# Kernel tuning notes

Measured on AMD Instinct MI355X. Metric: run time of the kernel, lower is better.

The kernel has to match this reference:

```python
import jax, jax.numpy as jnp
import numpy as np

L0, L1, L2 = 32, 16, 8
NS, NB = 512, 256
CUT = 7.0
N, E, G = 16384, 131072, 16
FEAT = L0 + 3 * L1 + 5 * L2  # 120


def setup_inputs() -> dict:
    key = jax.random.key(0)
    ks = jax.random.split(key, 16)
    rn = lambda k, s, sc=1.0: jax.random.normal(k, s, jnp.float32) * sc
    inp = {}
    inp['nodes'] = rn(ks[0], (N, FEAT))
    inp['pos'] = rn(ks[1], (N, 3)) * 5.0
    inp['cell'] = rn(ks[2], (G, 3, 3))
    inp['edge_shift'] = rn(ks[3], (E, 3))
    # tensor-product path weights (e3nn FullyConnectedTensorProduct, uvw mode)
    inp['W0'] = rn(ks[4], (L0, L0, NS))
    inp['W1'] = rn(ks[5], (L1, L1, NS))
    inp['W2'] = rn(ks[6], (L2, L2, NS))
    inp['ln_g'] = jnp.ones((NS,), jnp.float32)
    inp['ln_b'] = jnp.zeros((NS,), jnp.float32)
    inp['df_w1'] = rn(ks[7], (NB, 1024), NB ** -0.5)
    inp['df_b1'] = jnp.zeros((1024,), jnp.float32)
    inp['df_w2'] = rn(ks[8], (1024, NS), 1024 ** -0.5)
    inp['df_b2'] = jnp.zeros((NS,), jnp.float32)
    inp['mi_w1'] = rn(ks[9], (NS, 1024), NS ** -0.5)
    inp['mi_b1'] = jnp.zeros((1024,), jnp.float32)
    inp['mi_w2'] = rn(ks[10], (1024, 1024), 1024 ** -0.5)
    inp['mi_b2'] = jnp.zeros((1024,), jnp.float32)
    inp['mo_w'] = rn(ks[11], (1024, 1), 1024 ** -0.5)
    inp['mo_b'] = jnp.zeros((1,), jnp.float32)
    inp['edge_index'] = jax.random.randint(ks[12], (2, E), 0, N)
    inp['batch_vec'] = jnp.sort(jax.random.randint(ks[13], (N,), 0, G))
    return inp


def _split_irreps(x):
    x0 = x[:, :L0]                                   # (E, L0) scalars 0e
    x1 = x[:, L0:L0 + 3 * L1].reshape(-1, L1, 3)      # (E, L1, 3) vectors 1o
    x2 = x[:, L0 + 3 * L1:].reshape(-1, L2, 5)        # (E, L2, 5) 2e
    return x0, x1, x2


def reference(nodes, pos, cell, edge_shift, W0, W1, W2, ln_g, ln_b,
              df_w1, df_b1, df_w2, df_b2, mi_w1, mi_b1, mi_w2, mi_b2,
              mo_w, mo_b, edge_index, batch_vec):
    src, dst = edge_index[0], edge_index[1]
    # periodic-image translation vector per edge
    bcell = cell[batch_vec[src]]                      # (E,3,3)
    tvec = jnp.einsum('ei,eij->ej', edge_shift, bcell)
    radvec = pos[dst] - pos[src] + tvec               # (E,3)
    dist = jnp.linalg.norm(radvec, axis=1, keepdims=True)  # (E,1)
    r = 1.0 / (dist + 1e-6)
    # Bessel radial embedding with cutoff CUT, NB basis functions
    n = jnp.arange(1, NB + 1, dtype=jnp.float32)
    emb = jnp.sqrt(2.0 / CUT) * jnp.sin(n * jnp.pi * r / CUT) / r  # (E,NB)
    distfilter = jax.nn.silu(emb @ df_w1 + df_b1) @ df_w2 + df_b2  # (E,NS)

    # symmetrized fully-connected tensor product -> 0e scalars
    # 0.5*(tp(xs,xd)+tp(xd,xs)) == contraction of euv with symmetrized W
    xs0, xs1, xs2 = _split_irreps(nodes[src])
    xd0, xd1, xd2 = _split_irreps(nodes[dst])
    fan = jnp.sqrt(jnp.float32(L0 * L0 + L1 * L1 + L2 * L2))  # element path norm
    sym = lambda W: 0.5 * (W + W.transpose(1, 0, 2))
    e0 = jnp.einsum('eu,ev->euv', xs0, xd0)
    mixed = jnp.einsum('euv,uvw->ew', e0, sym(W0)) / fan
    e1 = jnp.einsum('eui,evi->euv', xs1, xd1)
    mixed = mixed + jnp.einsum('euv,uvw->ew', e1, sym(W1)) / (fan * jnp.sqrt(3.0))
    e2 = jnp.einsum('eui,evi->euv', xs2, xd2)
    mixed = mixed + jnp.einsum('euv,uvw->ew', e2, sym(W2)) / (fan * jnp.sqrt(5.0))

    # LayerNorm over numscalars
    mu = jnp.mean(mixed, axis=-1, keepdims=True)
    var = jnp.mean((mixed - mu) ** 2, axis=-1, keepdims=True)
    mixednorm = (mixed - mu) * jax.lax.rsqrt(var + 1e-5) * ln_g + ln_b

    reg = mixednorm * distfilter
    h = jax.nn.silu(reg @ mi_w1 + mi_b1)
    h = jax.nn.silu(h @ mi_w2 + mi_b2)
    return h @ mo_w + mo_b  # (E,1)
```

## Files before the change

kernel.cpp:

```cpp
#include <hip/hip_runtime.h>

#define EE 131072
#define NNODE 16384
#define FEAT 120
#define NS 512
#define NB 256
#define KCAT 1344

typedef unsigned short u16;
typedef __bf16 bf16x8 __attribute__((ext_vector_type(8)));
typedef float f32x4 __attribute__((ext_vector_type(4)));
typedef float f32x16 __attribute__((ext_vector_type(16)));
typedef unsigned short ushort8 __attribute__((ext_vector_type(8)));

__device__ __forceinline__ float b2f(u16 u) {
  union { unsigned int i; float f; } x; x.i = ((unsigned int)u) << 16; return x.f;
}
__device__ __forceinline__ u16 f2b(float f) {
  union { float f; unsigned int i; } x; x.f = f;
  unsigned int lsb = (x.i >> 16) & 1u;
  x.i += 0x7fffu + lsb;
  return (u16)(x.i >> 16);
}
__device__ __forceinline__ u16 f2b_fast(float f) {
  __bf16 h = (__bf16)f;
  union { __bf16 h; u16 u; } x; x.h = h; return x.u;
}
__device__ __forceinline__ float rdany(const void* p, long i, int f32) {
  return f32 ? ((const float*)p)[i] : b2f(((const u16*)p)[i]);
}

__device__ __forceinline__ void gload16(const u16* g, u16* l) {
  __builtin_amdgcn_global_load_lds(
      (__attribute__((address_space(1))) void*)(u16*)g,
      (__attribute__((address_space(3))) void*)l, 16, 0, 0);
}

__global__ void detect_k(const u16* __restrict__ nodes, int* __restrict__ flag) {
  __shared__ int cnt;
  if (threadIdx.x == 0) cnt = 0;
  __syncthreads();
  u16 v = nodes[threadIdx.x];
  int e = (v >> 7) & 0xFF;
  if (e >= 0x48) atomicAdd(&cnt, 1);
  __syncthreads();
  if (threadIdx.x == 0) *flag = (cnt >= 16) ? 1 : 0;
}

__global__ __launch_bounds__(256) void convert_k(const void* __restrict__ src,
                                                 u16* __restrict__ dst, long n,
                                                 const int* __restrict__ flag) {
  long i = (long)blockIdx.x * 256 + threadIdx.x;
  if (i >= n) return;
  if (*flag)
    dst[i] = f2b(((const float*)src)[i]);
  else
    dst[i] = ((const u16*)src)[i];
}

__global__ __launch_bounds__(256) void transpose_k(const u16* __restrict__ in,
                                                   u16* __restrict__ out, int R, int C) {
  __shared__ u16 tile[32][33];
  int c0 = blockIdx.x * 32, r0 = blockIdx.y * 32;
  int tx = threadIdx.x & 31, ty = threadIdx.x >> 5;
  for (int i = 0; i < 32; i += 8) {
    int r = r0 + ty + i, c = c0 + tx;
    if (r < R && c < C) tile[ty + i][tx] = in[(long)r * C + c];
  }
  __syncthreads();
  for (int i = 0; i < 32; i += 8) {
    int r = r0 + tx, c = c0 + ty + i;
    if (r < R && c < C) out[(long)c * R + r] = tile[tx][ty + i];
  }
}

__global__ __launch_bounds__(256) void build_wcat(const u16* __restrict__ W0,
                                                  const u16* __restrict__ W1,
                                                  const u16* __restrict__ W2,
                                                  u16* __restrict__ wcT) {
  int idx = blockIdx.x * 256 + threadIdx.x;
  if (idx >= NS * KCAT) return;
  int w = idx / KCAT, k = idx - w * KCAT;
  const float fan = 36.66060556f;
  float val;
  if (k < 1024) {
    int u = k >> 5, v = k & 31;
    val = 0.5f * (b2f(W0[(u * 32 + v) * NS + w]) + b2f(W0[(v * 32 + u) * NS + w])) / fan;
  } else if (k < 1280) {
    int j = k - 1024;
    int u = j >> 4, v = j & 15;
    val = 0.5f * (b2f(W1[(u * 16 + v) * NS + w]) + b2f(W1[(v * 16 + u) * NS + w])) /
          (fan * 1.7320508076f);
  } else {
    int j = k - 1280;
    int u = j >> 3, v = j & 7;
    val = 0.5f * (b2f(W2[(u * 8 + v) * NS + w]) + b2f(W2[(v * 8 + u) * NS + w])) /
          (fan * 2.2360679775f);
  }
  wcT[idx] = f2b(val);
}

__global__ __launch_bounds__(256) void edge_prep(
    const u16* __restrict__ nodes, const void* __restrict__ pos, const void* __restrict__ cell,
    const void* __restrict__ shift, const int* __restrict__ eidx, const int* __restrict__ batch,
    u16* __restrict__ emb, u16* __restrict__ ocat, int e0, const int* __restrict__ flag) {
  const int wave = threadIdx.x >> 6, lane = threadIdx.x & 63;
  const int el = blockIdx.x * 4 + wave;
  const int e = e0 + el;
  const int f32 = *flag;
  __shared__ u16 sxs[4][FEAT], sxd[4][FEAT];
  const int src = eidx[e], dst = eidx[EE + e];
  for (int i = lane; i < FEAT; i += 64) {
    sxs[wave][i] = nodes[(long)src * FEAT + i];
    sxd[wave][i] = nodes[(long)dst * FEAT + i];
  }
  __syncthreads();
  const int b = batch[src];
  float s0 = rdany(shift, (long)e * 3, f32), s1 = rdany(shift, (long)e * 3 + 1, f32),
        s2 = rdany(shift, (long)e * 3 + 2, f32);
  float d2 = 0.f;
#pragma unroll
  for (int j = 0; j < 3; j++) {
    float tv = s0 * rdany(cell, b * 9 + j, f32) + s1 * rdany(cell, b * 9 + 3 + j, f32) +
               s2 * rdany(cell, b * 9 + 6 + j, f32);
    float rv = rdany(pos, dst * 3 + j, f32) - rdany(pos, src * 3 + j, f32) + tv;
    d2 += rv * rv;
  }
  float dist = sqrtf(d2);
  float r = 1.0f / (dist + 1e-6f);
  const float c0 = 0.5345224838f;
  const float pi7 = 0.44879895051f;
#pragma unroll
  for (int j = 0; j < 4; j++) {
    int n = lane + 64 * j;
    float val = c0 * sinf((float)(n + 1) * pi7 * r) / r;
    emb[(long)el * NB + n] = f2b(val);
  }
  const u16* xs = sxs[wave];
  const u16* xd = sxd[wave];
  u16* orow = ocat + (long)el * KCAT;
#pragma unroll
  for (int j = 0; j < 16; j++) {
    int k = lane + 64 * j;
    int u = k >> 5, v = k & 31;
    orow[k] = f2b(b2f(xs[u]) * b2f(xd[v]));
  }
#pragma unroll
  for (int j = 0; j < 4; j++) {
    int k = lane + 64 * j;
    int u = k >> 4, v = k & 15;
    float s = 0.f;
#pragma unroll
    for (int i = 0; i < 3; i++) s += b2f(xs[32 + u * 3 + i]) * b2f(xd[32 + v * 3 + i]);
    orow[1024 + k] = f2b(s);
  }
  {
    int u = lane >> 3, v = lane & 7;
    float s = 0.f;
#pragma unroll
    for (int i = 0; i < 5; i++) s += b2f(xs[80 + u * 5 + i]) * b2f(xd[80 + v * 5 + i]);
    orow[1280 + lane] = f2b(s);
  }
}

template <int ACT, int OF32, int HEAD>
__global__ __launch_bounds__(256) void gemm_bt(const u16* __restrict__ A,
                                               const u16* __restrict__ BT,
                                               const u16* __restrict__ bias,
                                               void* __restrict__ Cv,
                                               const u16* __restrict__ hw,
                                               float* __restrict__ outf, int N, int K) {
  __shared__ __align__(16) u16 lA[128 * 64];
  __shared__ __align__(16) u16 lB[128 * 64];
  const int tid = threadIdx.x;
  const int wave = tid >> 6, lane = tid & 63;
  const int half = lane >> 5, l32 = lane & 31, r7 = lane & 7;

  const int nb_n = N >> 7;
  const int nb_m = gridDim.x / nb_n;
  int mi, ni;
  if ((nb_m & 7) == 0) {
    int f = blockIdx.x;
    int xcd = f & 7, s = f >> 3;
    int per = nb_m >> 3;
    mi = xcd * per + s / nb_n;
    ni = s - (s / nb_n) * nb_n;
  } else {
    mi = blockIdx.x / nb_n;
    ni = blockIdx.x - mi * nb_n;
  }
  const long m0 = (long)mi * 128;
  const int n0 = ni * 128;
  const int wm = (wave >> 1) * 64, wn = (wave & 1) * 64;

  f32x16 acc[2][2];
#pragma unroll
  for (int i = 0; i < 2; i++)
#pragma unroll
    for (int j = 0; j < 2; j++)
#pragma unroll
      for (int q = 0; q < 16; q++) acc[i][j][q] = 0.f;

  const int srow = tid >> 3;
  const int gseg = (tid & 7) ^ (srow & 7);
  const u16* Ag = A + (m0 + srow) * K + gseg * 8;
  const u16* Bg = BT + (long)(n0 + srow) * K + gseg * 8;
  u16* la = &lA[tid * 8];
  u16* lb = &lB[tid * 8];

  for (int k0 = 0; k0 < K; k0 += 64) {
#pragma unroll
    for (int ro = 0; ro < 4; ro++) gload16(Ag + (long)(ro * 32) * K + k0, la + ro * 2048);
#pragma unroll
    for (int ro = 0; ro < 4; ro++) gload16(Bg + (long)(ro * 32) * K + k0, lb + ro * 2048);
    __syncthreads();
#pragma unroll
    for (int s = 0; s < 4; s++) {
      const int sl = ((((s << 1) + half) ^ r7) << 3);
      bf16x8 a0 = *(const bf16x8*)&lA[(wm + l32) * 64 + sl];
      bf16x8 a1 = *(const bf16x8*)&lA[(wm + 32 + l32) * 64 + sl];
      bf16x8 b0 = *(const bf16x8*)&lB[(wn + l32) * 64 + sl];
      bf16x8 b1 = *(const bf16x8*)&lB[(wn + 32 + l32) * 64 + sl];
      acc[0][0] = __builtin_amdgcn_mfma_f32_32x32x16_bf16(a0, b0, acc[0][0], 0, 0, 0);
      acc[0][1] = __builtin_amdgcn_mfma_f32_32x32x16_bf16(a0, b1, acc[0][1], 0, 0, 0);
      acc[1][0] = __builtin_amdgcn_mfma_f32_32x32x16_bf16(a1, b0, acc[1][0], 0, 0, 0);
      acc[1][1] = __builtin_amdgcn_mfma_f32_32x32x16_bf16(a1, b1, acc[1][1], 0, 0, 0);
    }
    __syncthreads();
  }

  float* Cf = (float*)Cv;
  u16* Cb = (u16*)Cv;
  float rsum[2][16];
  if (HEAD) {
#pragma unroll
    for (int mt = 0; mt < 2; mt++)
#pragma unroll
      for (int rg = 0; rg < 16; rg++) rsum[mt][rg] = 0.f;
  }
#pragma unroll
  for (int mt = 0; mt < 2; mt++) {
#pragma unroll
    for (int nt = 0; nt < 2; nt++) {
      const int col = n0 + wn + nt * 32 + l32;
      float bv = bias ? b2f(bias[col]) : 0.0f;
      float hwv = HEAD ? b2f(hw[col]) : 0.f;
#pragma unroll
      for (int rg = 0; rg < 16; rg++) {
        long row = m0 + wm + mt * 32 + (rg & 3) + ((rg >> 2) << 3) + (half << 2);
        float v = acc[mt][nt][rg] + bv;
        if (ACT) v = __fdividef(v, 1.0f + __expf(-v));
        if (HEAD) {
          rsum[mt][rg] += v * hwv;
        } else if (OF32) {
          Cf[row * N + col] = v;
        } else {
          Cb[row * N + col] = f2b_fast(v);
        }
      }
    }
  }
  if (HEAD) {
#pragma unroll
    for (int mt = 0; mt < 2; mt++)
#pragma unroll
      for (int rg = 0; rg < 16; rg++) {
        float s = rsum[mt][rg];
        s += __shfl_xor(s, 1);
        s += __shfl_xor(s, 2);
        s += __shfl_xor(s, 4);
        s += __shfl_xor(s, 8);
        s += __shfl_xor(s, 16);
        if (l32 == 0) {
          long row = m0 + wm + mt * 32 + (rg & 3) + ((rg >> 2) << 3) + (half << 2);
          atomicAdd(&outf[row], s);
        }
      }
  }
}

__global__ __launch_bounds__(256) void ln_mul_k(const float* __restrict__ mixed,
                                                const u16* __restrict__ g,
                                                const u16* __restrict__ bvec,
                                                u16* __restrict__ dfreg) {
  const int wave = threadIdx.x >> 6, lane = threadIdx.x & 63;
  const long e = (long)blockIdx.x * 4 + wave;
  const float* row = mixed + e * NS;
  float x[8];
  f32x4 v0 = *(const f32x4*)&row[lane * 8];
  f32x4 v1 = *(const f32x4*)&row[lane * 8 + 4];
#pragma unroll
  for (int j = 0; j < 4; j++) { x[j] = v0[j]; x[4 + j] = v1[j]; }
  float s = 0.f, sq = 0.f;
#pragma unroll
  for (int j = 0; j < 8; j++) { s += x[j]; sq += x[j] * x[j]; }
  for (int o = 32; o; o >>= 1) { s += __shfl_xor(s, o); sq += __shfl_xor(sq, o); }
  float mu = s * (1.0f / 512.0f);
  float var = sq * (1.0f / 512.0f) - mu * mu;
  float rstd = rsqrtf(var + 1e-5f);
  u16* drow = dfreg + e * NS;
  ushort8 dv = *(const ushort8*)&drow[lane * 8];
  ushort8 ov;
#pragma unroll
  for (int j = 0; j < 8; j++) {
    int c = lane * 8 + j;
    float val = (x[j] - mu) * rstd * b2f(g[c]) + b2f(bvec[c]);
    ov[j] = f2b(val * b2f(dv[j]));
  }
  *(ushort8*)&drow[lane * 8] = ov;
}

__global__ __launch_bounds__(256) void head_finish(const float* __restrict__ outf,
                                                   const u16* __restrict__ b,
                                                   void* __restrict__ out,
                                                   const int* __restrict__ flag) {
  int e = blockIdx.x * 256 + threadIdx.x;
  float v = outf[e] + b2f(b[0]);
  if (*flag)
    ((float*)out)[e] = v;
  else
    ((u16*)out)[e] = f2b(v);
}

extern "C" void kernel_launch(void* const* d_in, const int* in_sizes, int n_in, void* d_out,
                              int out_size, void* d_ws, size_t ws_size, hipStream_t stream) {
  const int* eidx = (const int*)d_in[19];
  const int* batch = (const int*)d_in[20];

  char* ws = (char*)d_ws;
  size_t off = 0;
  auto alloc = [&](size_t bytes) {
    char* p = ws + off;
    off += (bytes + 255) & ~(size_t)255;
    return p;
  };

  int* flag = (int*)alloc(256);
  float* outf = (float*)alloc((size_t)EE * 4);

  detect_k<<<1, 256, 0, stream>>>((const u16*)d_in[0], flag);

  u16* cv[19];
  for (int i = 0; i < 19; i++) {
    long n = in_sizes[i];
    cv[i] = (u16*)alloc((size_t)n * 2);
    convert_k<<<(int)((n + 255) / 256), 256, 0, stream>>>(d_in[i], cv[i], n, flag);
  }
  const u16* nodes = cv[0];
  const u16* W0 = cv[4];
  const u16* W1 = cv[5];
  const u16* W2 = cv[6];
  const u16* ln_g = cv[7];
  const u16* ln_b = cv[8];
  const u16* df_w1 = cv[9];
  const u16* df_b1 = cv[10];
  const u16* df_w2 = cv[11];
  const u16* df_b2 = cv[12];
  const u16* mi_w1 = cv[13];
  const u16* mi_b1 = cv[14];
  const u16* mi_w2 = cv[15];
  const u16* mi_b2 = cv[16];
  const u16* mo_w = cv[17];
  const u16* mo_b = cv[18];

  u16* w1T = (u16*)alloc(1024 * 256 * 2);
  u16* w2T = (u16*)alloc(512 * 1024 * 2);
  u16* m1T = (u16*)alloc(1024 * 512 * 2);
  u16* m2T = (u16*)alloc((size_t)1024 * 1024 * 2);
  u16* wcT = (u16*)alloc((size_t)NS * KCAT * 2);

  int nchunk = 1;
  while (nchunk < 64) {
    size_t CHs = (size_t)(EE / nchunk);
    size_t need = off + CHs * 6272 + 8192;
    if (need <= ws_size) break;
    nchunk <<= 1;
  }
  const int CH = EE / nchunk;

  u16* ocat = (u16*)alloc((size_t)CH * KCAT * 2);
  u16* emb = (u16*)alloc((size_t)CH * NB * 2);
  u16* h1 = (u16*)alloc((size_t)CH * 1024 * 2);
  u16* dfb = (u16*)alloc((size_t)CH * NS * 2);
  u16* h2 = ocat;
  float* mixed = (float*)h1;

  transpose_k<<<dim3(1024 / 32, 256 / 32), 256, 0, stream>>>(df_w1, w1T, 256, 1024);
  transpose_k<<<dim3(512 / 32, 1024 / 32), 256, 0, stream>>>(df_w2, w2T, 1024, 512);
  transpose_k<<<dim3(1024 / 32, 512 / 32), 256, 0, stream>>>(mi_w1, m1T, 512, 1024);
  transpose_k<<<dim3(1024 / 32, 1024 / 32), 256, 0, stream>>>(mi_w2, m2T, 1024, 1024);
  build_wcat<<<(NS * KCAT + 255) / 256, 256, 0, stream>>>(W0, W1, W2, wcT);

  hipMemsetAsync(outf, 0, (size_t)EE * 4, stream);

  const int RB = CH / 128;
  for (int c = 0; c < nchunk; c++) {
    const int eb = c * CH;
    edge_prep<<<CH / 4, 256, 0, stream>>>(nodes, d_in[1], d_in[2], d_in[3], eidx, batch, emb,
                                          ocat, eb, flag);

    gemm_bt<1, 0, 0><<<RB * 8, 256, 0, stream>>>(emb, w1T, df_b1, h1, nullptr, nullptr, 1024, 256);
    gemm_bt<0, 0, 0><<<RB * 4, 256, 0, stream>>>(h1, w2T, df_b2, dfb, nullptr, nullptr, 512, 1024);

    gemm_bt<0, 1, 0><<<RB * 4, 256, 0, stream>>>(ocat, wcT, nullptr, mixed, nullptr, nullptr, 512,
                                                 1344);

    ln_mul_k<<<CH / 4, 256, 0, stream>>>(mixed, ln_g, ln_b, dfb);

    gemm_bt<1, 0, 0><<<RB * 8, 256, 0, stream>>>(dfb, m1T, mi_b1, h2, nullptr, nullptr, 1024, 512);
    gemm_bt<1, 0, 1><<<RB * 8, 256, 0, stream>>>(h2, m2T, mi_b2, nullptr, mo_w, outf + eb, 1024,
                                                 1024);
  }
  head_finish<<<EE / 256, 256, 0, stream>>>(outf, mo_b, d_out, flag);
}
```

Baseline: 1.651 ms.

## Rewrite GEMM as 256x256 tile, 8-wave, double-buffered pipelined MFMA kernel

Replaces the 128x128, 4-wave GEMM with a 256x256 tile computed by 8 waves. Each wave now holds a 128x64 accumulator. LDS is double-buffered and the A/B loads for the next K step are interleaved with MFMA phases, with s_setprio and explicit waitcnt and barriers. The XCD-aware block remap is simplified and the epilogue is adapted to the larger per-wave tile. This aims to raise data reuse per load and hide global latency behind compute. In exchange it uses much more LDS and registers per block, launches fewer blocks, and has intricate barrier ordering that could be fragile.

```diff
diff --git a/kernel.cpp b/kernel.cpp
--- a/kernel.cpp
+++ b/kernel.cpp
@@ -163,119 +163,205 @@
   }
 }
 
+#define STG_A(buf, h, kk)                                                        \
+  do {                                                                           \
+    gload16(Ag + ((h) * 128) * (long)K + (kk), &lA[buf][(h) * 8192 + tid * 8]);  \
+    gload16(Ag + ((h) * 128 + 64) * (long)K + (kk),                              \
+            &lA[buf][(h) * 8192 + 4096 + tid * 8]);                              \
+  } while (0)
+#define STG_B(buf, h, kk)                                                        \
+  do {                                                                           \
+    gload16(Bg + ((h) * 128) * (long)K + (kk), &lB[buf][(h) * 8192 + tid * 8]);  \
+    gload16(Bg + ((h) * 128 + 64) * (long)K + (kk),                              \
+            &lB[buf][(h) * 8192 + 4096 + tid * 8]);                              \
+  } while (0)
+#define RD_A(buf, fm, s)                                                         \
+  (*(const bf16x8*)&lA[buf][((wm * 128 + (fm)*32 + l32) << 6) +                  \
+                            ((((s)*2 + half) ^ r7) << 3)])
+#define RD_B(buf, fn, s)                                                         \
+  (*(const bf16x8*)&lB[buf][((wn * 64 + (fn)*32 + l32) << 6) +                   \
+                            ((((s)*2 + half) ^ r7) << 3)])
+#define MF(a, b, c) __builtin_amdgcn_mfma_f32_32x32x16_bf16(a, b, c, 0, 0, 0)
+
 template <int ACT, int OF32, int HEAD>
-__global__ __launch_bounds__(256) void gemm_bt(const u16* __restrict__ A,
-                                               const u16* __restrict__ BT,
-                                               const u16* __restrict__ bias,
-                                               void* __restrict__ Cv,
-                                               const u16* __restrict__ hw,
-                                               float* __restrict__ outf, int N, int K) {
-  __shared__ __align__(16) u16 lA[128 * 64];
-  __shared__ __align__(16) u16 lB[128 * 64];
+__global__ __launch_bounds__(512, 2) void gemm_bt(const u16* __restrict__ A,
+                                                  const u16* __restrict__ BT,
+                                                  const u16* __restrict__ bias,
+                                                  void* __restrict__ Cv,
+                                                  const u16* __restrict__ hw,
+                                                  float* __restrict__ outf, int N, int K) {
+  __shared__ __align__(16) u16 lA[2][256 * 64];
+  __shared__ __align__(16) u16 lB[2][256 * 64];
   const int tid = threadIdx.x;
-  const int wave = tid >> 6, lane = tid & 63;
+  const int lane = tid & 63;
+  const int wave = tid >> 6;
   const int half = lane >> 5, l32 = lane & 31, r7 = lane & 7;
-
-  const int nb_n = N >> 7;
-  const int nb_m = gridDim.x / nb_n;
-  int mi, ni;
-  if ((nb_m & 7) == 0) {
-    int f = blockIdx.x;
-    int xcd = f & 7, s = f >> 3;
-    int per = nb_m >> 3;
-    mi = xcd * per + s / nb_n;
-    ni = s - (s / nb_n) * nb_n;
-  } else {
-    mi = blockIdx.x / nb_n;
-    ni = blockIdx.x - mi * nb_n;
-  }
-  const long m0 = (long)mi * 128;
-  const int n0 = ni * 128;
-  const int wm = (wave >> 1) * 64, wn = (wave & 1) * 64;
-
-  f32x16 acc[2][2];
-#pragma unroll
-  for (int i = 0; i < 2; i++)
-#pragma unroll
-    for (int j = 0; j < 2; j++)
-#pragma unroll
-      for (int q = 0; q < 16; q++) acc[i][j][q] = 0.f;
+  const int wm = wave >> 2, wn = wave & 3;
+
+  const int nbn = N >> 8;
+  int idx = blockIdx.x;
+  if ((gridDim.x & 7) == 0) {
+    int per = gridDim.x >> 3;
+    idx = (blockIdx.x & 7) * per + (blockIdx.x >> 3);
+  }
+  const int mi = idx / nbn;
+  const int ni = idx - mi * nbn;
+  const long m0 = (long)mi * 256;
+  const int n0 = ni << 8;
+  const int nk = K >> 6;
 
   const int srow = tid >> 3;
   const int gseg = (tid & 7) ^ (srow & 7);
-  const u16* Ag = A + (m0 + srow) * K + gseg * 8;
+  const u16* Ag = A + (m0 + srow) * (long)K + gseg * 8;
   const u16* Bg = BT + (long)(n0 + srow) * K + gseg * 8;
-  u16* la = &lA[tid * 8];
-  u16* lb = &lB[tid * 8];
-
-  for (int k0 = 0; k0 < K; k0 += 64) {
-#pragma unroll
-    for (int ro = 0; ro < 4; ro++) gload16(Ag + (long)(ro * 32) * K + k0, la + ro * 2048);
-#pragma unroll
-    for (int ro = 0; ro < 4; ro++) gload16(Bg + (long)(ro * 32) * K + k0, lb + ro * 2048);
-    __syncthreads();
+
+  f32x16 acc[4][2];
+#pragma unroll
+  for (int i = 0; i < 4; i++)
+#pragma unroll
+    for (int j = 0; j < 2; j++)
+#pragma unroll
+      for (int q = 0; q < 16; q++) acc[i][j][q] = 0.f;
+
+  STG_A(0, 0, 0);
+  STG_A(0, 1, 0);
+  STG_B(0, 0, 0);
+  STG_B(0, 1, 0);
+  if (nk > 1) {
+    STG_B(1, 0, 64);
+    STG_B(1, 1, 64);
+    asm volatile("s_waitcnt vmcnt(4)" ::: "memory");
+  } else {
+    asm volatile("s_waitcnt vmcnt(0)" ::: "memory");
+  }
+  __builtin_amdgcn_s_barrier();
+
+  bf16x8 av[2][4], b0[4], b1[4];
+
+  for (int t = 0; t < nk; ++t) {
+    const int cur = t & 1, nxt = cur ^ 1;
+    const int kA = (t + 1) << 6;
+    const int kB = (t + 2) << 6;
+    const bool pA = (t + 1) < nk;
+    const bool pB = (t + 2) < nk;
+
 #pragma unroll
     for (int s = 0; s < 4; s++) {
-      const int sl = ((((s << 1) + half) ^ r7) << 3);
-      bf16x8 a0 = *(const bf16x8*)&lA[(wm + l32) * 64 + sl];
-      bf16x8 a1 = *(const bf16x8*)&lA[(wm + 32 + l32) * 64 + sl];
-      bf16x8 b0 = *(const bf16x8*)&lB[(wn + l32) * 64 + sl];
-      bf16x8 b1 = *(const bf16x8*)&lB[(wn + 32 + l32) * 64 + sl];
-      acc[0][0] = __builtin_amdgcn_mfma_f32_32x32x16_bf16(a0, b0, acc[0][0], 0, 0, 0);
-      acc[0][1] = __builtin_amdgcn_mfma_f32_32x32x16_bf16(a0, b1, acc[0][1], 0, 0, 0);
-      acc[1][0] = __builtin_amdgcn_mfma_f32_32x32x16_bf16(a1, b0, acc[1][0], 0, 0, 0);
-      acc[1][1] = __builtin_amdgcn_mfma_f32_32x32x16_bf16(a1, b1, acc[1][1], 0, 0, 0);
-    }
-    __syncthreads();
-  }
-
+      av[0][s] = RD_A(cur, 0, s);
+      av[1][s] = RD_A(cur, 1, s);
+      b0[s] = RD_B(cur, 0, s);
+    }
+    if (pA) STG_A(nxt, 0, kA);
+    __builtin_amdgcn_s_barrier();
+    asm volatile("s_waitcnt lgkmcnt(0)" ::: "memory");
+    __builtin_amdgcn_s_setprio(1);
+#pragma unroll
+    for (int s = 0; s < 4; s++) {
+      acc[0][0] = MF(av[0][s], b0[s], acc[0][0]);
+      acc[1][0] = MF(av[1][s], b0[s], acc[1][0]);
+    }
+    __builtin_amdgcn_s_setprio(0);
+    __builtin_amdgcn_s_barrier();
+
+#pragma unroll
+    for (int s = 0; s < 4; s++) b1[s] = RD_B(cur, 1, s);
+    if (pA) STG_A(nxt, 1, kA);
+    __builtin_amdgcn_s_barrier();
+    asm volatile("s_waitcnt lgkmcnt(0)" ::: "memory");
+    __builtin_amdgcn_s_setprio(1);
+#pragma unroll
+    for (int s = 0; s < 4; s++) {
+      acc[0][1] = MF(av[0][s], b1[s], acc[0][1]);
+      acc[1][1] = MF(av[1][s], b1[s], acc[1][1]);
+    }
+    __builtin_amdgcn_s_setprio(0);
+    __builtin_amdgcn_s_barrier();
+
+#pragma unroll
+    for (int s = 0; s < 4; s++) {
+      av[0][s] = RD_A(cur, 2, s);
+      av[1][s] = RD_A(cur, 3, s);
+    }
+    if (pB) STG_B(cur, 0, kB);
+    __builtin_amdgcn_s_barrier();
+    asm volatile("s_waitcnt lgkmcnt(0)" ::: "memory");
+    __builtin_amdgcn_s_setprio(1);
+#pragma unroll
+    for (int s = 0; s < 4; s++) {
+      acc[2][0] = MF(av[0][s], b0[s], acc[2][0]);
+      acc[3][0] = MF(av[1][s], b0[s], acc[3][0]);
+    }
+    __builtin_amdgcn_s_setprio(0);
+    __builtin_amdgcn_s_barrier();
+
+    if (pB) {
+      STG_B(cur, 1, kB);
+      asm volatile("s_waitcnt vmcnt(4)" ::: "memory");
+    } else {
+      asm volatile("s_waitcnt vmcnt(0)" ::: "memory");
+    }
+    __builtin_amdgcn_s_barrier();
+    __builtin_amdgcn_s_setprio(1);
+#pragma unroll
+    for (int s = 0; s < 4; s++) {
+      acc[2][1] = MF(av[0][s], b1[s], acc[2][1]);
+      acc[3][1] = MF(av[1][s], b1[s], acc[3][1]);
+    }
+    __builtin_amdgcn_s_setprio(0);
+    __builtin_amdgcn_s_barrier();
+  }
+
+  const int colb = n0 + wn * 64 + l32;
   float* Cf = (float*)Cv;
   u16* Cb = (u16*)Cv;
-  float rsum[2][16];
   if (HEAD) {
-#pragma unroll
-    for (int mt = 0; mt < 2; mt++)
-#pragma unroll
-      for (int rg = 0; rg < 16; rg++) rsum[mt][rg] = 0.f;
-  }
-#pragma unroll
-  for (int mt = 0; mt < 2; mt++) {
-#pragma unroll
-    for (int nt = 0; nt < 2; nt++) {
-      const int col = n0 + wn + nt * 32 + l32;
-      float bv = bias ? b2f(bias[col]) : 0.0f;
-      float hwv = HEAD ? b2f(hw[col]) : 0.f;
+    const float bv0 = b2f(bias[colb]), bv1 = b2f(bias[colb + 32]);
+    const float hw0 = b2f(hw[colb]), hw1 = b2f(hw[colb + 32]);
+#pragma unroll
+    for (int fm = 0; fm < 4; fm++) {
 #pragma unroll
       for (int rg = 0; rg < 16; rg++) {
-        long row = m0 + wm + mt * 32 + (rg & 3) + ((rg >> 2) << 3) + (half << 2);
-        float v = acc[mt][nt][rg] + bv;
-        if (ACT) v = __fdividef(v, 1.0f + __expf(-v));
-        if (HEAD) {
-          rsum[mt][rg] += v * hwv;
-        } else if (OF32) {
-          Cf[row * N + col] = v;
-        } else {
-          Cb[row * N + col] = f2b_fast(v);
+        float v0 = acc[fm][0][rg] + bv0;
+        float v1 = acc[fm][1][rg] + bv1;
+        if (ACT) {
+          v0 = __fdividef(v0, 1.0f + __expf(-v0));
+          v1 = __fdividef(v1, 1.0f + __expf(-v1));
         }
-      }
-    }
-  }
-  if (HEAD) {
-#pragma unroll
-    for (int mt = 0; mt < 2; mt++)
-#pragma unroll
-      for (int rg = 0; rg < 16; rg++) {
-        float s = rsum[mt][rg];
+        float s = v0 * hw0 + v1 * hw1;
         s += __shfl_xor(s, 1);
         s += __shfl_xor(s, 2);
         s += __shfl_xor(s, 4);
         s += __shfl_xor(s, 8);
         s += __shfl_xor(s, 16);
         if (l32 == 0) {
-          long row = m0 + wm + mt * 32 + (rg & 3) + ((rg >> 2) << 3) + (half << 2);
+          long row = m0 + wm * 128 + fm * 32 + (rg & 3) + ((rg >> 2) << 3) + (half << 2);
           atomicAdd(&outf[row], s);
         }
       }
+    }
+  } else {
+    const float bv0 = bias ? b2f(bias[colb]) : 0.0f;
+    const float bv1 = bias ? b2f(bias[colb + 32]) : 0.0f;
+#pragma unroll
+    for (int fm = 0; fm < 4; fm++) {
+#pragma unroll
+      for (int rg = 0; rg < 16; rg++) {
+        long row = m0 + wm * 128 + fm * 32 + (rg & 3) + ((rg >> 2) << 3) + (half << 2);
+        float v0 = acc[fm][0][rg] + bv0;
+        float v1 = acc[fm][1][rg] + bv1;
+        if (ACT) {
+          v0 = __fdividef(v0, 1.0f + __expf(-v0));
+          v1 = __fdividef(v1, 1.0f + __expf(-v1));
+        }
+        if (OF32) {
+          Cf[row * N + colb] = v0;
+          Cf[row * N + colb + 32] = v1;
+        } else {
+          Cb[row * N + colb] = f2b_fast(v0);
+          Cb[row * N + colb + 32] = f2b_fast(v1);
+        }
+      }
+    }
   }
 }
 
@@ -393,22 +479,22 @@
 
   hipMemsetAsync(outf, 0, (size_t)EE * 4, stream);
 
-  const int RB = CH / 128;
+  const int RB = CH / 256;
   for (int c = 0; c < nchunk; c++) {
     const int eb = c * CH;
     edge_prep<<<CH / 4, 256, 0, stream>>>(nodes, d_in[1], d_in[2], d_in[3], eidx, batch, emb,
                                           ocat, eb, flag);
 
-    gemm_bt<1, 0, 0><<<RB * 8, 256, 0, stream>>>(emb, w1T, df_b1, h1, nullptr, nullptr, 1024, 256);
-    gemm_bt<0, 0, 0><<<RB * 4, 256, 0, stream>>>(h1, w2T, df_b2, dfb, nullptr, nullptr, 512, 1024);
-
-    gemm_bt<0, 1, 0><<<RB * 4, 256, 0, stream>>>(ocat, wcT, nullptr, mixed, nullptr, nullptr, 512,
+    gemm_bt<1, 0, 0><<<RB * 4, 512, 0, stream>>>(emb, w1T, df_b1, h1, nullptr, nullptr, 1024, 256);
+    gemm_bt<0, 0, 0><<<RB * 2, 512, 0, stream>>>(h1, w2T, df_b2, dfb, nullptr, nullptr, 512, 1024);
+
+    gemm_bt<0, 1, 0><<<RB * 2, 512, 0, stream>>>(ocat, wcT, nullptr, mixed, nullptr, nullptr, 512,
                                                  1344);
 
     ln_mul_k<<<CH / 4, 256, 0, stream>>>(mixed, ln_g, ln_b, dfb);
 
-    gemm_bt<1, 0, 0><<<RB * 8, 256, 0, stream>>>(dfb, m1T, mi_b1, h2, nullptr, nullptr, 1024, 512);
-    gemm_bt<1, 0, 1><<<RB * 8, 256, 0, stream>>>(h2, m2T, mi_b2, nullptr, mo_w, outf + eb, 1024,
+    gemm_bt<1, 0, 0><<<RB * 4, 512, 0, stream>>>(dfb, m1T, mi_b1, h2, nullptr, nullptr, 1024, 512);
+    gemm_bt<1, 0, 1><<<RB * 4, 512, 0, stream>>>(h2, m2T, mi_b2, nullptr, mo_w, outf + eb, 1024,
                                                  1024);
   }
   head_finish<<<EE / 256, 256, 0, stream>>>(outf, mo_b, d_out, flag);
```

Result: faster. 1.475 ms (-10.7%).
